# Kernel tuning notes

Measured on AMD Instinct MI355X. Metric: run time of the kernel, lower is better.

## Reference

```python
import jax, jax.numpy as jnp
import numpy as np

B, S, D, H = 2, 2048, 1024, 8
DH = D // H          # hidden_dim == attn_dim == 128
TOTAL = 4 * D        # (2*hidden_dim + 2*attn_dim) * H
EPS = 1e-5
ROPE_BASE = 10000.0


def _layernorm(x, g, b):
    m = jnp.mean(x, axis=-1, keepdims=True)
    v = jnp.mean(jnp.square(x - m), axis=-1, keepdims=True)
    return (x - m) * jax.lax.rsqrt(v + EPS) * g + b


def _rope(x):
    # x: [B, H, S, DH], interleaved even/odd RoPE as in the torch module
    half = DH // 2
    inv_freq = 1.0 / (ROPE_BASE ** (jnp.arange(0, DH, 2, dtype=jnp.float32) / DH))  # [half]
    t = jnp.arange(x.shape[2], dtype=jnp.float32)
    freqs = t[:, None] * inv_freq[None, :]                 # [S, half]
    cos = jnp.cos(freqs)[None, None, :, :]                 # [1,1,S,half]
    sin = jnp.sin(freqs)[None, None, :, :]
    xe, xo = x[..., 0::2], x[..., 1::2]
    re = xe * cos - xo * sin
    ro = xe * sin + xo * cos
    return jnp.stack([re, ro], axis=-1).reshape(x.shape)


def setup_inputs() -> dict:
    key = jax.random.key(0)
    ks = jax.random.split(key, 6)
    x = jax.random.normal(ks[0], (B, S, D), dtype=jnp.float32)
    attention_mask = jnp.ones((B, S), dtype=bool)
    # weights stored [in, out] so forward is x @ W + b
    w_uvqk = 0.02 * jax.random.normal(ks[1], (D, TOTAL), dtype=jnp.float32)
    b_uvqk = jnp.zeros((TOTAL,), dtype=jnp.float32)
    w_out = 0.02 * jax.random.normal(ks[2], (3 * D, D), dtype=jnp.float32)
    b_out = jnp.zeros((D,), dtype=jnp.float32)
    ln1_g = jnp.ones((D,), dtype=jnp.float32)
    ln1_b = jnp.zeros((D,), dtype=jnp.float32)
    ln2_g = jnp.ones((D,), dtype=jnp.float32)
    ln2_b = jnp.zeros((D,), dtype=jnp.float32)
    return {"x": x, "attention_mask": attention_mask,
            "ln1_g": ln1_g, "ln1_b": ln1_b,
            "w_uvqk": w_uvqk, "b_uvqk": b_uvqk,
            "ln2_g": ln2_g, "ln2_b": ln2_b,
            "w_out": w_out, "b_out": b_out}


def reference(x, attention_mask, ln1_g, ln1_b, w_uvqk, b_uvqk, ln2_g, ln2_b, w_out, b_out):
    normed = _layernorm(x, ln1_g, ln1_b)
    uvqk = jax.nn.silu(normed @ w_uvqk + b_uvqk)          # [B,S,4D]
    u, v, q, k = jnp.split(uvqk, [D, 2 * D, 3 * D], axis=-1)
    q = q.reshape(B, S, H, DH).transpose(0, 2, 1, 3)      # [B,H,S,DH]
    k = k.reshape(B, S, H, DH).transpose(0, 2, 1, 3)
    v = v.reshape(B, S, H, DH).transpose(0, 2, 1, 3)
    q, k = _rope(q), _rope(k)
    scale = jnp.float32(DH) ** 0.5
    scores = jnp.einsum('bhsd,bhtd->bhst', q, k) / scale  # [B,H,S,S] fp32
    causal = jnp.tril(jnp.ones((S, S), dtype=bool))
    pad = attention_mask[:, None, :, None] & attention_mask[:, None, None, :]
    valid = pad & causal[None, None, :, :]
    scores = jnp.where(valid, scores, jnp.float32(-30.0))
    scores = jnp.clip(scores, -30.0, 30.0)
    attn = jax.nn.silu(scores)                            # SiLU instead of softmax
    ao = jnp.einsum('bhst,bhtd->bhsd', attn, v)           # [B,H,S,DH]
    ao = ao.transpose(0, 2, 1, 3).reshape(B, S, D)
    normed_attn = _layernorm(ao, ln2_g, ln2_b)
    cat = jnp.concatenate([u, ao, normed_attn * u], axis=-1)  # [B,S,3D]
    return x + (cat @ w_out + b_out)
```

## Files before the change

### kernel.cpp

```cpp
#include <hip/hip_runtime.h>
#include <hip/hip_bf16.h>
#include <math.h>

#define Bm 2
#define Sm 2048
#define Dm 1024
#define Hm 8
#define DHm 128
#define TOTALm 4096
#define ROWS (Bm*Sm)
#define K2m (3*Dm)

typedef __bf16 bf16;
typedef __bf16 bf16x8 __attribute__((ext_vector_type(8)));
typedef __bf16 bf16x4 __attribute__((ext_vector_type(4)));
typedef float  f32x4  __attribute__((ext_vector_type(4)));

__device__ __forceinline__ void stage_tile_128x32(
    const bf16* __restrict__ g, int ld, bf16* lds, int tid)
{
    int wid = tid >> 6;
    #pragma unroll
    for (int j = 0; j < 2; j++) {
        int e0  = (j*256 + tid) * 8;
        int row = e0 >> 5, col = e0 & 31;
        const bf16* src = g + (size_t)row*ld + col;
        bf16* dst = lds + (size_t)(j*256 + wid*64)*8;
        __builtin_amdgcn_global_load_lds(
            (const __attribute__((address_space(1))) unsigned int*)src,
            (__attribute__((address_space(3))) unsigned int*)dst,
            16, 0, 0);
    }
}

__device__ __forceinline__ void stage_tile_64x32(
    const bf16* __restrict__ g, int ld, bf16* lds, int tid)
{
    int wid = tid >> 6;
    int e0 = tid * 8;
    int row = e0 >> 5, col = e0 & 31;
    const bf16* src = g + (size_t)row*ld + col;
    bf16* dst = lds + (size_t)wid*512;
    __builtin_amdgcn_global_load_lds(
        (const __attribute__((address_space(1))) unsigned int*)src,
        (__attribute__((address_space(3))) unsigned int*)dst,
        16, 0, 0);
}

__global__ __launch_bounds__(256) void ln1_kernel(
    const float* __restrict__ x, const float* __restrict__ g,
    const float* __restrict__ bb, bf16* __restrict__ out)
{
    int row = blockIdx.x;
    const float* xr = x + (size_t)row * Dm;
    int tid = threadIdx.x;
    float4 v = *(const float4*)(xr + tid*4);
    float s = v.x+v.y+v.z+v.w;
    for (int o=32;o>0;o>>=1) s += __shfl_down(s,o);
    __shared__ float red[4]; __shared__ float stats[2];
    int wid = tid>>6, lane = tid&63;
    if (lane==0) red[wid]=s;
    __syncthreads();
    if (tid==0) stats[0] = (red[0]+red[1]+red[2]+red[3]) * (1.f/Dm);
    __syncthreads();
    float m = stats[0];
    float d0=v.x-m,d1=v.y-m,d2=v.z-m,d3=v.w-m;
    float q = d0*d0+d1*d1+d2*d2+d3*d3;
    for (int o=32;o>0;o>>=1) q += __shfl_down(q,o);
    if (lane==0) red[wid]=q;
    __syncthreads();
    if (tid==0) stats[1] = rsqrtf((red[0]+red[1]+red[2]+red[3])*(1.f/Dm) + 1e-5f);
    __syncthreads();
    float rs = stats[1];
    float4 gv = *(const float4*)(g + tid*4);
    float4 bv = *(const float4*)(bb + tid*4);
    bf16x4 o;
    o[0] = (bf16)(d0*rs*gv.x + bv.x);
    o[1] = (bf16)(d1*rs*gv.y + bv.y);
    o[2] = (bf16)(d2*rs*gv.z + bv.z);
    o[3] = (bf16)(d3*rs*gv.w + bv.w);
    *(bf16x4*)(out + (size_t)row*Dm + tid*4) = o;
}

__global__ __launch_bounds__(256) void transpose_kernel(
    const float* __restrict__ in, bf16* __restrict__ out, int R, int C)
{
    __shared__ float tile[32][33];
    int c0 = blockIdx.x*32, r0 = blockIdx.y*32;
    int tx = threadIdx.x & 31, ty = threadIdx.x >> 5;
    for (int i=0;i<4;i++) {
        int r = ty + i*8;
        tile[r][tx] = in[(size_t)(r0+r)*C + c0+tx];
    }
    __syncthreads();
    for (int i=0;i<4;i++) {
        int cl = ty + i*8;
        out[(size_t)(c0+cl)*R + r0+tx] = (bf16)tile[tx][cl];
    }
}

__global__ __launch_bounds__(256) void rope_table_kernel(float* __restrict__ ct, float* __restrict__ st)
{
    int idx = blockIdx.x*256 + threadIdx.x;
    int t = idx >> 6, p = idx & 63;
    float inv = expf(-0.143911568f * (float)p);
    float f = (float)t * inv;
    float sv, cv;
    sincosf(f, &sv, &cv);
    ct[idx] = cv; st[idx] = sv;
}

__global__ __launch_bounds__(256,4) void gemm1_kernel(
    const bf16* __restrict__ A, const bf16* __restrict__ Bt,
    const float* __restrict__ bias,
    const float* __restrict__ ct, const float* __restrict__ st,
    bf16* __restrict__ cat, bf16* __restrict__ qb, bf16* __restrict__ kb,
    bf16* __restrict__ vt)
{
    __shared__ __align__(16) bf16 sm[17408];
    const int K = Dm;
    int m0 = blockIdx.y*128, n0 = blockIdx.x*128;
    int tid = threadIdx.x, wid = tid>>6, lane = tid&63;
    int quad = lane>>4, l16 = lane&15;
    int wm = (wid>>1)*64, wn = (wid&1)*64;
    f32x4 acc[4][4] = {};
    bf16* sA = sm;
    bf16* sB = sm + 8192;
    for (int k0=0;k0<K;k0+=64) {
        __syncthreads();
        stage_tile_128x32(A  + (size_t)m0*K + k0,      K, sA,        tid);
        stage_tile_128x32(A  + (size_t)m0*K + k0 + 32, K, sA + 4096, tid);
        stage_tile_128x32(Bt + (size_t)n0*K + k0,      K, sB,        tid);
        stage_tile_128x32(Bt + (size_t)n0*K + k0 + 32, K, sB + 4096, tid);
        __syncthreads();
        #pragma unroll
        for (int kc=0;kc<2;kc++) {
            bf16x8 af[4], bfr[4];
            #pragma unroll
            for (int t=0;t<4;t++) af[t]  = *(const bf16x8*)&sA[kc*4096 + (wm+t*16+l16)*32 + quad*8];
            #pragma unroll
            for (int t=0;t<4;t++) bfr[t] = *(const bf16x8*)&sB[kc*4096 + (wn+t*16+l16)*32 + quad*8];
            #pragma unroll
            for (int tm=0;tm<4;tm++)
                #pragma unroll
                for (int tn=0;tn<4;tn++)
                    acc[tm][tn] = __builtin_amdgcn_mfma_f32_16x16x32_bf16(af[tm], bfr[tn], acc[tm][tn], 0,0,0);
        }
    }
    int sect = n0 >> 10;
    if (sect == 1) {
        __syncthreads();
        #pragma unroll
        for (int tm=0;tm<4;tm++)
        #pragma unroll
        for (int tn=0;tn<4;tn++) {
            int colg = n0 + wn + tn*16 + l16;
            float bval = bias[colg];
            int d = colg & 127;
            #pragma unroll
            for (int r=0;r<4;r++) {
                int srow = wm + tm*16 + quad*4 + r;
                float val = acc[tm][tn][r] + bval;
                val = val / (1.f + __expf(-val));
                sm[d*136 + srow] = (bf16)val;
            }
        }
        __syncthreads();
        int h = (n0 >> 7) & 7;
        int b = m0 >> 11, s0l = m0 & 2047;
        int d2 = tid >> 1, sh = (tid & 1)*64;
        bf16* dst = vt + ((size_t)(b*Hm+h)*DHm + d2)*Sm + s0l + sh;
        const bf16* srcl = &sm[d2*136 + sh];
        #pragma unroll
        for (int i=0;i<8;i++)
            *(bf16x8*)(dst + i*8) = *(const bf16x8*)(srcl + i*8);
    } else if (sect == 0) {
        #pragma unroll
        for (int tm=0;tm<4;tm++)
        #pragma unroll
        for (int tn=0;tn<4;tn++) {
            int c = n0 + wn + tn*16 + l16;
            float bval = bias[c];
            #pragma unroll
            for (int r=0;r<4;r++) {
                int row = m0 + wm + tm*16 + quad*4 + r;
                float val = acc[tm][tn][r] + bval;
                val = val / (1.f + __expf(-val));
                cat[(size_t)row*K2m + c] = (bf16)val;
            }
        }
    } else {
        bf16* dstb = (sect==2) ? qb : kb;
        float postscale = (sect==2) ? 0.08838834764831845f : 1.0f;
        #pragma unroll
        for (int tm=0;tm<4;tm++)
        #pragma unroll
        for (int tn=0;tn<4;tn++) {
            int colg = n0 + wn + tn*16 + l16;
            int c = colg & 1023;
            int h = c>>7, d = c&127, p = d>>1;
            float bval = bias[colg];
            #pragma unroll
            for (int r=0;r<4;r++) {
                int row = m0 + wm + tm*16 + quad*4 + r;
                float val = acc[tm][tn][r] + bval;
                val = val / (1.f + __expf(-val));
                int b = row>>11, s = row&2047;
                float pv = __shfl_xor(val, 1);
                float cv = ct[s*64+p], sv = st[s*64+p];
                float res = (d&1) ? (pv*sv + val*cv) : (val*cv - pv*sv);
                dstb[((size_t)(b*Hm+h)*Sm + s)*DHm + d] = (bf16)(res * postscale);
            }
        }
    }
}

__global__ __launch_bounds__(256,2) void attn_kernel(
    const bf16* __restrict__ qb, const bf16* __restrict__ kb,
    const bf16* __restrict__ vt, float* __restrict__ ao0,
    float* __restrict__ ao1)
{
    __shared__ __align__(16) bf16 sK[16384];
    __shared__ __align__(16) bf16 P[64*136];
    int bid = blockIdx.x;
    int head = bid & 15;
    int idx = bid >> 4;
    int b = head >> 3, h = head & 7;
    int qt, k_begin, k_end;
    float* aoOut;
    if (idx < 32) {
        qt = 31 - (idx >> 1);
        int nkt = (qt >> 1) + 1;
        int half = (nkt + 1) >> 1;
        if ((idx & 1) == 0) { k_begin = 0;    k_end = half; aoOut = ao0; }
        else                { k_begin = half; k_end = nkt;  aoOut = ao1; }
    } else {
        qt = 47 - idx;
        k_begin = 0; k_end = (qt >> 1) + 1;
        aoOut = ao0;
    }
    const size_t headoff = (size_t)(b*Hm+h)*Sm*DHm;
    const bf16* Q  = qb + headoff;
    const bf16* Km = kb + headoff;
    const bf16* V  = vt + headoff;
    int tid=threadIdx.x, wid=tid>>6, lane=tid&63, quad=lane>>4, l16=lane&15;
    int wm=(wid>>1)*32, wn=(wid&1)*64;
    int q0 = qt*64;
    f32x4 accO[2][4] = {};
    bf16x8 qf[4][2];
    #pragma unroll
    for (int kc=0;kc<4;kc++)
        #pragma unroll
        for (int t=0;t<2;t++)
            qf[kc][t] = *(const bf16x8*)(Q + (size_t)(q0+wm+t*16+l16)*DHm + kc*32 + quad*8);
    int e0 = tid*8, e1 = (256+tid)*8;
    int kr0 = e0>>5, kcol0 = e0&31;
    int kr1 = e1>>5, kcol1 = e1&31;
    bf16x8 kreg[4][2];
    {
        int t0 = k_begin*128;
        #pragma unroll
        for (int kc=0;kc<4;kc++) {
            kreg[kc][0] = *(const bf16x8*)(Km + (size_t)(t0+kr0)*DHm + kc*32 + kcol0);
            kreg[kc][1] = *(const bf16x8*)(Km + (size_t)(t0+kr1)*DHm + kc*32 + kcol1);
        }
    }
    for (int kt=k_begin; kt<k_end; kt++) {
        int t0 = kt*128;
        __syncthreads();
        #pragma unroll
        for (int kc=0;kc<4;kc++) {
            *(bf16x8*)&sK[kc*4096 + e0] = kreg[kc][0];
            *(bf16x8*)&sK[kc*4096 + e1] = kreg[kc][1];
        }
        __syncthreads();
        if (kt+1 < k_end) {
            int t0n = t0 + 128;
            #pragma unroll
            for (int kc=0;kc<4;kc++) {
                kreg[kc][0] = *(const bf16x8*)(Km + (size_t)(t0n+kr0)*DHm + kc*32 + kcol0);
                kreg[kc][1] = *(const bf16x8*)(Km + (size_t)(t0n+kr1)*DHm + kc*32 + kcol1);
            }
        }
        bf16x8 vreg[4][4];
        #pragma unroll
        for (int kc=0;kc<4;kc++)
            #pragma unroll
            for (int t=0;t<4;t++)
                vreg[kc][t] = *(const bf16x8*)(V + (size_t)(wn+t*16+l16)*Sm + t0 + kc*32 + quad*8);
        f32x4 accS[2][4] = {};
        #pragma unroll
        for (int kc=0;kc<4;kc++) {
            bf16x8 bfr[4];
            #pragma unroll
            for (int t=0;t<4;t++) bfr[t] = *(const bf16x8*)&sK[kc*4096 + (wn+t*16+l16)*32 + quad*8];
            #pragma unroll
            for (int tm=0;tm<2;tm++)
                #pragma unroll
                for (int tn=0;tn<4;tn++)
                    accS[tm][tn] = __builtin_amdgcn_mfma_f32_16x16x32_bf16(qf[kc][tm], bfr[tn], accS[tm][tn], 0,0,0);
        }
        if (t0 + 127 <= q0) {
            #pragma unroll
            for (int tm=0;tm<2;tm++)
            #pragma unroll
            for (int tn=0;tn<4;tn++)
                #pragma unroll
                for (int r=0;r<4;r++) {
                    int srow = wm+tm*16+quad*4+r;
                    int tcol = wn+tn*16+l16;
                    float s = fminf(30.f, fmaxf(-30.f, accS[tm][tn][r]));
                    float p = s * __builtin_amdgcn_rcpf(1.f + __expf(-s));
                    P[srow*136 + tcol] = (bf16)p;
                }
        } else {
            #pragma unroll
            for (int tm=0;tm<2;tm++)
            #pragma unroll
            for (int tn=0;tn<4;tn++)
                #pragma unroll
                for (int r=0;r<4;r++) {
                    int srow = wm+tm*16+quad*4+r;
                    int tcol = wn+tn*16+l16;
                    float s = fminf(30.f, fmaxf(-30.f, accS[tm][tn][r]));
                    float p = (t0+tcol > q0+srow) ? 0.f
                              : s * __builtin_amdgcn_rcpf(1.f + __expf(-s));
                    P[srow*136 + tcol] = (bf16)p;
                }
        }
        __syncthreads();
        int kcn = ((q0 + 63 - t0) >> 5) + 1;
        if (kcn > 4) kcn = 4;
        #pragma unroll
        for (int kc=0;kc<4;kc++) {
            if (kc >= kcn) break;
            bf16x8 af[2];
            #pragma unroll
            for (int t=0;t<2;t++) af[t] = *(const bf16x8*)&P[(wm+t*16+l16)*136 + kc*32 + quad*8];
            #pragma unroll
            for (int tm=0;tm<2;tm++)
                #pragma unroll
                for (int tn=0;tn<4;tn++)
                    accO[tm][tn] = __builtin_amdgcn_mfma_f32_16x16x32_bf16(af[tm], vreg[kc][tn], accO[tm][tn], 0,0,0);
        }
    }
    #pragma unroll
    for (int tm=0;tm<2;tm++)
    #pragma unroll
    for (int tn=0;tn<4;tn++)
        #pragma unroll
        for (int r=0;r<4;r++) {
            int s = q0+wm+tm*16+quad*4+r;
            int d = wn+tn*16+l16;
            aoOut[((size_t)(b*Sm+s))*Dm + h*DHm + d] = accO[tm][tn][r];
        }
}

__global__ __launch_bounds__(256) void ln2_cat_kernel(
    const float* __restrict__ ao0, const float* __restrict__ ao1,
    const float* __restrict__ g,
    const float* __restrict__ bb, bf16* __restrict__ cat)
{
    int row = blockIdx.x;
    int tid = threadIdx.x;
    float4 v  = *(const float4*)(ao0 + (size_t)row*Dm + tid*4);
    float4 v1 = *(const float4*)(ao1 + (size_t)row*Dm + tid*4);
    v.x += v1.x; v.y += v1.y; v.z += v1.z; v.w += v1.w;
    float s = v.x+v.y+v.z+v.w;
    for (int o=32;o>0;o>>=1) s += __shfl_down(s,o);
    __shared__ float red[4]; __shared__ float stats[2];
    int wid = tid>>6, lane = tid&63;
    if (lane==0) red[wid]=s;
    __syncthreads();
    if (tid==0) stats[0] = (red[0]+red[1]+red[2]+red[3]) * (1.f/Dm);
    __syncthreads();
    float m = stats[0];
    float d0=v.x-m,d1=v.y-m,d2=v.z-m,d3=v.w-m;
    float q = d0*d0+d1*d1+d2*d2+d3*d3;
    for (int o=32;o>0;o>>=1) q += __shfl_down(q,o);
    if (lane==0) red[wid]=q;
    __syncthreads();
    if (tid==0) stats[1] = rsqrtf((red[0]+red[1]+red[2]+red[3])*(1.f/Dm) + 1e-5f);
    __syncthreads();
    float rs = stats[1];
    float4 gv = *(const float4*)(g + tid*4);
    float4 bv = *(const float4*)(bb + tid*4);
    bf16* crow = cat + (size_t)row * K2m;
    bf16x4 u4 = *(const bf16x4*)(crow + tid*4);
    bf16x4 a4, nu4;
    a4[0]=(bf16)v.x; a4[1]=(bf16)v.y; a4[2]=(bf16)v.z; a4[3]=(bf16)v.w;
    nu4[0]=(bf16)(((v.x-m)*rs*gv.x+bv.x) * (float)u4[0]);
    nu4[1]=(bf16)(((v.y-m)*rs*gv.y+bv.y) * (float)u4[1]);
    nu4[2]=(bf16)(((v.z-m)*rs*gv.z+bv.z) * (float)u4[2]);
    nu4[3]=(bf16)(((v.w-m)*rs*gv.w+bv.w) * (float)u4[3]);
    *(bf16x4*)(crow + 1024 + tid*4) = a4;
    *(bf16x4*)(crow + 2048 + tid*4) = nu4;
}

__global__ __launch_bounds__(256,4) void gemm2_kernel(
    const bf16* __restrict__ A, const bf16* __restrict__ Bt,
    const float* __restrict__ bias, const float* __restrict__ x,
    float* __restrict__ out)
{
    __shared__ __align__(16) bf16 sm[12288];
    const int K = K2m, N = Dm;
    int m0 = blockIdx.y*128, n0 = blockIdx.x*64;
    int tid = threadIdx.x, wid = tid>>6, lane = tid&63;
    int quad = lane>>4, l16 = lane&15;
    int wm = (wid>>1)*64, wn = (wid&1)*32;
    f32x4 acc[4][2] = {};
    bf16* sA = sm;
    bf16* sB = sm + 8192;
    for (int k0=0;k0<K;k0+=64) {
        __syncthreads();
        stage_tile_128x32(A  + (size_t)m0*K + k0,      K, sA,        tid);
        stage_tile_128x32(A  + (size_t)m0*K + k0 + 32, K, sA + 4096, tid);
        stage_tile_64x32 (Bt + (size_t)n0*K + k0,      K, sB,        tid);
        stage_tile_64x32 (Bt + (size_t)n0*K + k0 + 32, K, sB + 2048, tid);
        __syncthreads();
        #pragma unroll
        for (int kc=0;kc<2;kc++) {
            bf16x8 af[4], bfr[2];
            #pragma unroll
            for (int t=0;t<4;t++) af[t]  = *(const bf16x8*)&sA[kc*4096 + (wm+t*16+l16)*32 + quad*8];
            #pragma unroll
            for (int t=0;t<2;t++) bfr[t] = *(const bf16x8*)&sB[kc*2048 + (wn+t*16+l16)*32 + quad*8];
            #pragma unroll
            for (int tm=0;tm<4;tm++)
                #pragma unroll
                for (int tn=0;tn<2;tn++)
                    acc[tm][tn] = __builtin_amdgcn_mfma_f32_16x16x32_bf16(af[tm], bfr[tn], acc[tm][tn], 0,0,0);
        }
    }
    #pragma unroll
    for (int tm=0;tm<4;tm++)
    #pragma unroll
    for (int tn=0;tn<2;tn++) {
        int col = n0 + wn + tn*16 + l16;
        float bval = bias[col];
        #pragma unroll
        for (int r=0;r<4;r++) {
            int row = m0 + wm + tm*16 + quad*4 + r;
            out[(size_t)row*N + col] = acc[tm][tn][r] + bval + x[(size_t)row*N + col];
        }
    }
}

extern "C" void kernel_launch(void* const* d_in, const int* in_sizes, int n_in,
                              void* d_out, int out_size, void* d_ws, size_t ws_size,
                              hipStream_t stream)
{
    const float* x      = (const float*)d_in[0];
    const float* ln1_g  = (const float*)d_in[2];
    const float* ln1_b  = (const float*)d_in[3];
    const float* w_uvqk = (const float*)d_in[4];
    const float* b_uvqk = (const float*)d_in[5];
    const float* ln2_g  = (const float*)d_in[6];
    const float* ln2_b  = (const float*)d_in[7];
    const float* w_out  = (const float*)d_in[8];
    const float* b_out  = (const float*)d_in[9];

    char* w = (char*)d_ws;
    bf16*  normed = (bf16*)(w);
    bf16*  Wt1    = (bf16*)(w + 8388608);
    bf16*  Wt2    = (bf16*)(w + 16777216);
    bf16*  qb     = (bf16*)(w + 23068672);
    bf16*  kb     = (bf16*)(w + 31457280);
    bf16*  vt     = (bf16*)(w + 39845888);
    float* ao0    = (float*)(w + 48234496);
    bf16*  cat    = (bf16*)(w + 65011712);
    float* ct     = (float*)(w + 90177536);
    float* st     = (float*)(w + 90701824);
    float* ao1    = (float*)(w);

    ln1_kernel<<<ROWS, 256, 0, stream>>>(x, ln1_g, ln1_b, normed);
    transpose_kernel<<<dim3(TOTALm/32, Dm/32), 256, 0, stream>>>(w_uvqk, Wt1, Dm, TOTALm);
    transpose_kernel<<<dim3(Dm/32, K2m/32), 256, 0, stream>>>(w_out, Wt2, K2m, Dm);
    rope_table_kernel<<<(Sm*64)/256, 256, 0, stream>>>(ct, st);
    gemm1_kernel<<<dim3(TOTALm/128, ROWS/128), 256, 0, stream>>>(
        normed, Wt1, b_uvqk, ct, st, cat, qb, kb, vt);
    hipMemsetAsync(ao1, 0, (size_t)ROWS*Dm*sizeof(float), stream);
    attn_kernel<<<768, 256, 0, stream>>>(qb, kb, vt, ao0, ao1);
    ln2_cat_kernel<<<ROWS, 256, 0, stream>>>(ao0, ao1, ln2_g, ln2_b, cat);
    gemm2_kernel<<<dim3(Dm/64, ROWS/128), 256, 0, stream>>>(
        cat, Wt2, b_out, x, (float*)d_out);
}
```

Baseline: 283.4 us.

## Merge prep kernels into one launch and restructure attention loop for occupancy

Merges the LN1, two weight transposes and the RoPE table kernels into a single prep_kernel launch, dispatching on block index. This removes three kernel launches and their gaps. In attention, V fragments are now loaded inside the PV loop rather than prefetched for all chunks, and scores are computed one 16-column strip at a time. The unified causal mask branch and smaller live register set allow raising launch bounds to 3 blocks per SM. The trade-off is less latency hiding for V loads, plus a possible register spill or reduced unrolling from the dynamic PV loop.

```diff
diff --git a/kernel.cpp b/kernel.cpp
--- a/kernel.cpp
+++ b/kernel.cpp
@@ -47,67 +47,70 @@
         16, 0, 0);
 }
 
-__global__ __launch_bounds__(256) void ln1_kernel(
-    const float* __restrict__ x, const float* __restrict__ g,
-    const float* __restrict__ bb, bf16* __restrict__ out)
-{
-    int row = blockIdx.x;
-    const float* xr = x + (size_t)row * Dm;
+__global__ __launch_bounds__(256) void prep_kernel(
+    const float* __restrict__ x, const float* __restrict__ g1,
+    const float* __restrict__ b1, bf16* __restrict__ normed,
+    const float* __restrict__ w_uvqk, bf16* __restrict__ Wt1,
+    const float* __restrict__ w_out,  bf16* __restrict__ Wt2,
+    float* __restrict__ ct, float* __restrict__ st)
+{
+    __shared__ float tile[32][33];
+    __shared__ float red[4];
+    __shared__ float stats[2];
+    int bid = blockIdx.x;
     int tid = threadIdx.x;
-    float4 v = *(const float4*)(xr + tid*4);
-    float s = v.x+v.y+v.z+v.w;
-    for (int o=32;o>0;o>>=1) s += __shfl_down(s,o);
-    __shared__ float red[4]; __shared__ float stats[2];
-    int wid = tid>>6, lane = tid&63;
-    if (lane==0) red[wid]=s;
-    __syncthreads();
-    if (tid==0) stats[0] = (red[0]+red[1]+red[2]+red[3]) * (1.f/Dm);
-    __syncthreads();
-    float m = stats[0];
-    float d0=v.x-m,d1=v.y-m,d2=v.z-m,d3=v.w-m;
-    float q = d0*d0+d1*d1+d2*d2+d3*d3;
-    for (int o=32;o>0;o>>=1) q += __shfl_down(q,o);
-    if (lane==0) red[wid]=q;
-    __syncthreads();
-    if (tid==0) stats[1] = rsqrtf((red[0]+red[1]+red[2]+red[3])*(1.f/Dm) + 1e-5f);
-    __syncthreads();
-    float rs = stats[1];
-    float4 gv = *(const float4*)(g + tid*4);
-    float4 bv = *(const float4*)(bb + tid*4);
-    bf16x4 o;
-    o[0] = (bf16)(d0*rs*gv.x + bv.x);
-    o[1] = (bf16)(d1*rs*gv.y + bv.y);
-    o[2] = (bf16)(d2*rs*gv.z + bv.z);
-    o[3] = (bf16)(d3*rs*gv.w + bv.w);
-    *(bf16x4*)(out + (size_t)row*Dm + tid*4) = o;
-}
-
-__global__ __launch_bounds__(256) void transpose_kernel(
-    const float* __restrict__ in, bf16* __restrict__ out, int R, int C)
-{
-    __shared__ float tile[32][33];
-    int c0 = blockIdx.x*32, r0 = blockIdx.y*32;
-    int tx = threadIdx.x & 31, ty = threadIdx.x >> 5;
-    for (int i=0;i<4;i++) {
-        int r = ty + i*8;
-        tile[r][tx] = in[(size_t)(r0+r)*C + c0+tx];
-    }
-    __syncthreads();
-    for (int i=0;i<4;i++) {
-        int cl = ty + i*8;
-        out[(size_t)(c0+cl)*R + r0+tx] = (bf16)tile[tx][cl];
-    }
-}
-
-__global__ __launch_bounds__(256) void rope_table_kernel(float* __restrict__ ct, float* __restrict__ st)
-{
-    int idx = blockIdx.x*256 + threadIdx.x;
-    int t = idx >> 6, p = idx & 63;
-    float inv = expf(-0.143911568f * (float)p);
-    float f = (float)t * inv;
-    float sv, cv;
-    sincosf(f, &sv, &cv);
-    ct[idx] = cv; st[idx] = sv;
+    if (bid < 7168) {
+        const float* in; bf16* out; int R, C, bx, by;
+        if (bid < 4096) { in = w_uvqk; out = Wt1; R = Dm;  C = TOTALm; bx = bid & 127; by = bid >> 7; }
+        else { int id2 = bid - 4096; in = w_out; out = Wt2; R = K2m; C = Dm; bx = id2 & 31; by = id2 >> 5; }
+        int c0 = bx*32, r0 = by*32;
+        int tx = tid & 31, ty = tid >> 5;
+        for (int i=0;i<4;i++) {
+            int r = ty + i*8;
+            tile[r][tx] = in[(size_t)(r0+r)*C + c0+tx];
+        }
+        __syncthreads();
+        for (int i=0;i<4;i++) {
+            int cl = ty + i*8;
+            out[(size_t)(c0+cl)*R + r0+tx] = (bf16)tile[tx][cl];
+        }
+    } else if (bid < 7680) {
+        int idx = (bid - 7168)*256 + tid;
+        int t = idx >> 6, p = idx & 63;
+        float inv = expf(-0.143911568f * (float)p);
+        float f = (float)t * inv;
+        float sv, cv;
+        sincosf(f, &sv, &cv);
+        ct[idx] = cv; st[idx] = sv;
+    } else {
+        int row = bid - 7680;
+        const float* xr = x + (size_t)row * Dm;
+        float4 v = *(const float4*)(xr + tid*4);
+        float s = v.x+v.y+v.z+v.w;
+        for (int o=32;o>0;o>>=1) s += __shfl_down(s,o);
+        int wid = tid>>6, lane = tid&63;
+        if (lane==0) red[wid]=s;
+        __syncthreads();
+        if (tid==0) stats[0] = (red[0]+red[1]+red[2]+red[3]) * (1.f/Dm);
+        __syncthreads();
+        float m = stats[0];
+        float d0=v.x-m,d1=v.y-m,d2=v.z-m,d3=v.w-m;
+        float q = d0*d0+d1*d1+d2*d2+d3*d3;
+        for (int o=32;o>0;o>>=1) q += __shfl_down(q,o);
+        if (lane==0) red[wid]=q;
+        __syncthreads();
+        if (tid==0) stats[1] = rsqrtf((red[0]+red[1]+red[2]+red[3])*(1.f/Dm) + 1e-5f);
+        __syncthreads();
+        float rs = stats[1];
+        float4 gv = *(const float4*)(g1 + tid*4);
+        float4 bv = *(const float4*)(b1 + tid*4);
+        bf16x4 o;
+        o[0] = (bf16)(d0*rs*gv.x + bv.x);
+        o[1] = (bf16)(d1*rs*gv.y + bv.y);
+        o[2] = (bf16)(d2*rs*gv.z + bv.z);
+        o[3] = (bf16)(d3*rs*gv.w + bv.w);
+        *(bf16x4*)(normed + (size_t)row*Dm + tid*4) = o;
+    }
 }
 
 __global__ __launch_bounds__(256,4) void gemm1_kernel(
@@ -215,7 +218,7 @@
     }
 }
 
-__global__ __launch_bounds__(256,2) void attn_kernel(
+__global__ __launch_bounds__(256,3) void attn_kernel(
     const bf16* __restrict__ qb, const bf16* __restrict__ kb,
     const bf16* __restrict__ vt, float* __restrict__ ao0,
     float* __restrict__ ao1)
@@ -282,66 +285,43 @@
                 kreg[kc][1] = *(const bf16x8*)(Km + (size_t)(t0n+kr1)*DHm + kc*32 + kcol1);
             }
         }
-        bf16x8 vreg[4][4];
-        #pragma unroll
-        for (int kc=0;kc<4;kc++)
-            #pragma unroll
-            for (int t=0;t<4;t++)
-                vreg[kc][t] = *(const bf16x8*)(V + (size_t)(wn+t*16+l16)*Sm + t0 + kc*32 + quad*8);
-        f32x4 accS[2][4] = {};
-        #pragma unroll
-        for (int kc=0;kc<4;kc++) {
-            bf16x8 bfr[4];
-            #pragma unroll
-            for (int t=0;t<4;t++) bfr[t] = *(const bf16x8*)&sK[kc*4096 + (wn+t*16+l16)*32 + quad*8];
+        bool clean = (t0 + 127 <= q0);
+        #pragma unroll
+        for (int ts=0; ts<4; ts++) {
+            f32x4 accS[2] = {};
+            #pragma unroll
+            for (int kc=0;kc<4;kc++) {
+                bf16x8 bfr = *(const bf16x8*)&sK[kc*4096 + (wn+ts*16+l16)*32 + quad*8];
+                #pragma unroll
+                for (int tm=0;tm<2;tm++)
+                    accS[tm] = __builtin_amdgcn_mfma_f32_16x16x32_bf16(qf[kc][tm], bfr, accS[tm], 0,0,0);
+            }
+            #pragma unroll
+            for (int tm=0;tm<2;tm++)
+                #pragma unroll
+                for (int r=0;r<4;r++) {
+                    int srow = wm+tm*16+quad*4+r;
+                    int tcol = wn+ts*16+l16;
+                    float s = fminf(30.f, fmaxf(-30.f, accS[tm][r]));
+                    float p = s * __builtin_amdgcn_rcpf(1.f + __expf(-s));
+                    if (!clean && (t0+tcol > q0+srow)) p = 0.f;
+                    P[srow*136 + tcol] = (bf16)p;
+                }
+        }
+        __syncthreads();
+        int kcn = ((q0 + 63 - t0) >> 5) + 1;
+        if (kcn > 4) kcn = 4;
+        for (int kc=0;kc<kcn;kc++) {
+            bf16x8 af[2], bfr[4];
+            #pragma unroll
+            for (int t=0;t<2;t++) af[t]  = *(const bf16x8*)&P[(wm+t*16+l16)*136 + kc*32 + quad*8];
+            #pragma unroll
+            for (int t=0;t<4;t++) bfr[t] = *(const bf16x8*)(V + (size_t)(wn+t*16+l16)*Sm + t0 + kc*32 + quad*8);
             #pragma unroll
             for (int tm=0;tm<2;tm++)
                 #pragma unroll
                 for (int tn=0;tn<4;tn++)
-                    accS[tm][tn] = __builtin_amdgcn_mfma_f32_16x16x32_bf16(qf[kc][tm], bfr[tn], accS[tm][tn], 0,0,0);
-        }
-        if (t0 + 127 <= q0) {
-            #pragma unroll
-            for (int tm=0;tm<2;tm++)
-            #pragma unroll
-            for (int tn=0;tn<4;tn++)
-                #pragma unroll
-                for (int r=0;r<4;r++) {
-                    int srow = wm+tm*16+quad*4+r;
-                    int tcol = wn+tn*16+l16;
-                    float s = fminf(30.f, fmaxf(-30.f, accS[tm][tn][r]));
-                    float p = s * __builtin_amdgcn_rcpf(1.f + __expf(-s));
-                    P[srow*136 + tcol] = (bf16)p;
-                }
-        } else {
-            #pragma unroll
-            for (int tm=0;tm<2;tm++)
-            #pragma unroll
-            for (int tn=0;tn<4;tn++)
-                #pragma unroll
-                for (int r=0;r<4;r++) {
-                    int srow = wm+tm*16+quad*4+r;
-                    int tcol = wn+tn*16+l16;
-                    float s = fminf(30.f, fmaxf(-30.f, accS[tm][tn][r]));
-                    float p = (t0+tcol > q0+srow) ? 0.f
-                              : s * __builtin_amdgcn_rcpf(1.f + __expf(-s));
-                    P[srow*136 + tcol] = (bf16)p;
-                }
-        }
-        __syncthreads();
-        int kcn = ((q0 + 63 - t0) >> 5) + 1;
-        if (kcn > 4) kcn = 4;
-        #pragma unroll
-        for (int kc=0;kc<4;kc++) {
-            if (kc >= kcn) break;
-            bf16x8 af[2];
-            #pragma unroll
-            for (int t=0;t<2;t++) af[t] = *(const bf16x8*)&P[(wm+t*16+l16)*136 + kc*32 + quad*8];
-            #pragma unroll
-            for (int tm=0;tm<2;tm++)
-                #pragma unroll
-                for (int tn=0;tn<4;tn++)
-                    accO[tm][tn] = __builtin_amdgcn_mfma_f32_16x16x32_bf16(af[tm], vreg[kc][tn], accO[tm][tn], 0,0,0);
+                    accO[tm][tn] = __builtin_amdgcn_mfma_f32_16x16x32_bf16(af[tm], bfr[tn], accO[tm][tn], 0,0,0);
         }
     }
     #pragma unroll
@@ -473,10 +453,8 @@
     float* st     = (float*)(w + 90701824);
     float* ao1    = (float*)(w);
 
-    ln1_kernel<<<ROWS, 256, 0, stream>>>(x, ln1_g, ln1_b, normed);
-    transpose_kernel<<<dim3(TOTALm/32, Dm/32), 256, 0, stream>>>(w_uvqk, Wt1, Dm, TOTALm);
-    transpose_kernel<<<dim3(Dm/32, K2m/32), 256, 0, stream>>>(w_out, Wt2, K2m, Dm);
-    rope_table_kernel<<<(Sm*64)/256, 256, 0, stream>>>(ct, st);
+    prep_kernel<<<11776, 256, 0, stream>>>(x, ln1_g, ln1_b, normed,
+                                           w_uvqk, Wt1, w_out, Wt2, ct, st);
     gemm1_kernel<<<dim3(TOTALm/128, ROWS/128), 256, 0, stream>>>(
         normed, Wt1, b_uvqk, ct, st, cat, qb, kb, vt);
     hipMemsetAsync(ao1, 0, (size_t)ROWS*Dm*sizeof(float), stream);
```

Result: faster. 269.4 us (-5.0%).
